# Kernel tuning notes

Hardware: AMD Instinct MI355X
Metric: run time of the kernel (lower is better)

Reference implementation:

```python
import jax, jax.numpy as jnp
import numpy as np

B, H, W = 16, 544, 960
DISP_MAX = 64.0


def setup_inputs() -> dict:
    key = jax.random.key(0)
    k1, k2, k3, k4 = jax.random.split(key, 4)
    dl = jax.random.uniform(k1, (B, 1, H, W), dtype=jnp.float32) * DISP_MAX
    seg_r = jax.random.normal(k2, (B, 1, H, W), dtype=jnp.float32)
    dlgt = jax.random.uniform(k3, (B, H, W), dtype=jnp.float32) * DISP_MAX
    lgt = jax.random.normal(k4, (B, 1, H, W), dtype=jnp.float32)
    return {"dl": dl, "seg_r": seg_r, "dlgt": dlgt, "lgt": lgt}


def _warp(x, disp):
    """Disparity warp: sample x at (h, w - disp) with horizontal bilinear
    interpolation and zeros padding (grid_sample equivalent; y is untouched
    so the vertical weights collapse to 1)."""
    Bc, C, Hc, Wc = x.shape
    cols = jnp.arange(Wc, dtype=x.dtype)  # [W]
    sx = cols[None, None, None, :] - disp  # [B,1,H,W] sampling x-coord
    x0 = jnp.floor(sx)
    wx = sx - x0  # fractional part, carries grad wrt disp
    x0i = x0.astype(jnp.int32)
    x1i = x0i + 1
    v0m = ((x0i >= 0) & (x0i < Wc)).astype(x.dtype)
    v1m = ((x1i >= 0) & (x1i < Wc)).astype(x.dtype)
    x0c = jnp.clip(x0i, 0, Wc - 1)
    x1c = jnp.clip(x1i, 0, Wc - 1)
    # gather along width; C == 1 broadcasts against disp's channel dim
    g0 = jnp.take_along_axis(x, jnp.broadcast_to(x0c, x.shape), axis=-1)
    g1 = jnp.take_along_axis(x, jnp.broadcast_to(x1c, x.shape), axis=-1)
    return (1.0 - wx) * g0 * v0m + wx * g1 * v1m


def _smooth_l1(d):
    ad = jnp.abs(d)
    return jnp.where(ad < 1.0, 0.5 * d * d, ad - 0.5)


def reference(dl, seg_r, dlgt, lgt):
    mask = lgt > 0  # [B,1,H,W] bool
    mf = mask.astype(dl.dtype)
    cnt = mf.sum()
    recon_l = jax.nn.sigmoid(_warp(seg_r, dl))
    # masked-mean smooth L1 == mean over boolean-selected elements
    loss_recon = (_smooth_l1(recon_l - lgt) * mf).sum() / cnt
    loss = (_smooth_l1(dl - dlgt[:, None, :, :]) * mf).sum() / cnt
    loss = jnp.where(jnp.isnan(loss), jnp.zeros_like(loss), loss)
    return loss + 0.5 * loss_recon
```

## Files before the change

kernel.cpp:

```cpp
#include <hip/hip_runtime.h>
#include <math.h>

#define W 960
#define NTOT (16 * 544 * 960)
#define N4 (NTOT / 4)
#define TPB 256
#define NBLOCKS 2048

typedef float vfloat4 __attribute__((ext_vector_type(4)));

__device__ __forceinline__ float smooth_l1f(float d) {
    float ad = fabsf(d);
    return ad < 1.0f ? 0.5f * d * d : ad - 0.5f;
}

__global__ __launch_bounds__(TPB) void loss_kernel(
    const float* __restrict__ dl,
    const float* __restrict__ seg_r,
    const float* __restrict__ dlgt,
    const float* __restrict__ lgt,
    double* __restrict__ ws)
{
    const int tid = threadIdx.x;
    float cnt = 0.f, s_loss = 0.f, s_recon = 0.f;

    for (int i4 = blockIdx.x * TPB + tid; i4 < N4; i4 += NBLOCKS * TPB) {
        int i  = i4 << 2;
        int w0 = i % W;
        const float* __restrict__ row = seg_r + (i - w0);

        vfloat4 d4 = __builtin_nontemporal_load((const vfloat4*)dl   + i4);
        vfloat4 l4 = __builtin_nontemporal_load((const vfloat4*)lgt  + i4);
        vfloat4 t4 = __builtin_nontemporal_load((const vfloat4*)dlgt + i4);

        #pragma unroll
        for (int k = 0; k < 4; ++k) {
            float lv = l4[k];
            float m = lv > 0.f ? 1.f : 0.f;
            cnt += m;
            float d = d4[k];
            s_loss += m * smooth_l1f(d - t4[k]);

            float sx  = (float)(w0 + k) - d;
            float x0f = floorf(sx);
            float wx  = sx - x0f;
            int x0 = (int)x0f;
            int x1 = x0 + 1;
            float m0 = (x0 >= 0 && x0 < W) ? 1.f : 0.f;
            float m1 = (x1 >= 0 && x1 < W) ? 1.f : 0.f;
            int x0c = min(max(x0, 0), W - 1);
            int x1c = min(max(x1, 0), W - 1);
            float g0 = row[x0c] * m0;
            float g1 = row[x1c] * m1;
            float wv = fmaf(wx, g1 - g0, g0);
            float recon = 1.f / (1.f + __expf(-wv));
            s_recon += m * smooth_l1f(recon - lv);
        }
    }

    double dc = (double)cnt, dlo = (double)s_loss, dre = (double)s_recon;
    for (int off = 32; off > 0; off >>= 1) {
        dc  += __shfl_down(dc,  off, 64);
        dlo += __shfl_down(dlo, off, 64);
        dre += __shfl_down(dre, off, 64);
    }
    __shared__ double sh[3][TPB / 64];
    int lane = tid & 63, wid = tid >> 6;
    if (lane == 0) { sh[0][wid] = dc; sh[1][wid] = dlo; sh[2][wid] = dre; }
    __syncthreads();

    if (tid == 0) {
        double c = 0, l = 0, r = 0;
        #pragma unroll
        for (int j = 0; j < TPB / 64; ++j) { c += sh[0][j]; l += sh[1][j]; r += sh[2][j]; }
        double* slot = ws + blockIdx.x * 4;
        slot[0] = c; slot[1] = l; slot[2] = r;
    }
}

__global__ __launch_bounds__(256) void finalize_kernel(
    const double* __restrict__ ws, float* __restrict__ out)
{
    double c = 0, l = 0, r = 0;
    for (int i = threadIdx.x; i < NBLOCKS; i += 256) {
        const double* slot = ws + i * 4;
        c += slot[0]; l += slot[1]; r += slot[2];
    }
    for (int off = 32; off > 0; off >>= 1) {
        c += __shfl_down(c, off, 64);
        l += __shfl_down(l, off, 64);
        r += __shfl_down(r, off, 64);
    }
    __shared__ double sh[3][4];
    int lane = threadIdx.x & 63, wid = threadIdx.x >> 6;
    if (lane == 0) { sh[0][wid] = c; sh[1][wid] = l; sh[2][wid] = r; }
    __syncthreads();
    if (threadIdx.x == 0) {
        double cc = 0, ll = 0, rr = 0;
        #pragma unroll
        for (int j = 0; j < 4; ++j) { cc += sh[0][j]; ll += sh[1][j]; rr += sh[2][j]; }
        double loss = ll / cc;
        if (isnan(loss)) loss = 0.0;
        out[0] = (float)(loss + 0.5 * (rr / cc));
    }
}

extern "C" void kernel_launch(void* const* d_in, const int* in_sizes, int n_in,
                              void* d_out, int out_size, void* d_ws, size_t ws_size,
                              hipStream_t stream) {
    const float* dl    = (const float*)d_in[0];
    const float* seg_r = (const float*)d_in[1];
    const float* dlgt  = (const float*)d_in[2];
    const float* lgt   = (const float*)d_in[3];
    double* ws = (double*)d_ws;

    loss_kernel<<<NBLOCKS, TPB, 0, stream>>>(dl, seg_r, dlgt, lgt, ws);
    finalize_kernel<<<1, 256, 0, stream>>>(ws, (float*)d_out);
}
```

Measured before the change: 149.1 us.

## Stage seg_r rows in LDS with one wave per row for warp gathers

Each wave now owns one image row and copies that seg_r row into shared memory, so the bilinear gathers read LDS instead of scattered global/cache loads. The grid-stride flat loop becomes a fixed per-row mapping with 2176 blocks, and the two gathers use one clamped adjacent pair with selects in place of two independent clamps. The main loads drop from float4 nontemporal to scalar coalesced loads, which may raise the instruction count, and the larger block count changes how the reduction is partitioned.

```diff
diff --git a/kernel.cpp b/kernel.cpp
--- a/kernel.cpp
+++ b/kernel.cpp
@@ -2,10 +2,9 @@
 #include <math.h>
 
 #define W 960
-#define NTOT (16 * 544 * 960)
-#define N4 (NTOT / 4)
+#define NROWS (16 * 544)
 #define TPB 256
-#define NBLOCKS 2048
+#define NBLOCKS (NROWS / 4)
 
 typedef float vfloat4 __attribute__((ext_vector_type(4)));
 
@@ -21,41 +20,49 @@
     const float* __restrict__ lgt,
     double* __restrict__ ws)
 {
-    const int tid = threadIdx.x;
+    __shared__ float srow[4][W];
+    __shared__ double sh[3][4];
+    const int tid  = threadIdx.x;
+    const int lane = tid & 63;
+    const int wave = tid >> 6;
+    const int rb   = (blockIdx.x * 4 + wave) * W;
+
+    #pragma unroll
+    for (int j = 0; j < 4; ++j) {
+        int idx4 = lane + 64 * j;
+        if (idx4 < 240)
+            *(vfloat4*)&srow[wave][idx4 << 2] = *(const vfloat4*)(seg_r + rb + (idx4 << 2));
+    }
+
+    const float* __restrict__ srw = srow[wave];
     float cnt = 0.f, s_loss = 0.f, s_recon = 0.f;
 
-    for (int i4 = blockIdx.x * TPB + tid; i4 < N4; i4 += NBLOCKS * TPB) {
-        int i  = i4 << 2;
-        int w0 = i % W;
-        const float* __restrict__ row = seg_r + (i - w0);
+    #pragma unroll
+    for (int j = 0; j < 15; ++j) {
+        int col = lane + 64 * j;
+        float d  = dl  [rb + col];
+        float lv = lgt [rb + col];
+        float tv = dlgt[rb + col];
 
-        vfloat4 d4 = __builtin_nontemporal_load((const vfloat4*)dl   + i4);
-        vfloat4 l4 = __builtin_nontemporal_load((const vfloat4*)lgt  + i4);
-        vfloat4 t4 = __builtin_nontemporal_load((const vfloat4*)dlgt + i4);
+        float m = lv > 0.f ? 1.f : 0.f;
+        cnt += m;
+        s_loss += m * smooth_l1f(d - tv);
 
-        #pragma unroll
-        for (int k = 0; k < 4; ++k) {
-            float lv = l4[k];
-            float m = lv > 0.f ? 1.f : 0.f;
-            cnt += m;
-            float d = d4[k];
-            s_loss += m * smooth_l1f(d - t4[k]);
-
-            float sx  = (float)(w0 + k) - d;
-            float x0f = floorf(sx);
-            float wx  = sx - x0f;
-            int x0 = (int)x0f;
-            int x1 = x0 + 1;
-            float m0 = (x0 >= 0 && x0 < W) ? 1.f : 0.f;
-            float m1 = (x1 >= 0 && x1 < W) ? 1.f : 0.f;
-            int x0c = min(max(x0, 0), W - 1);
-            int x1c = min(max(x1, 0), W - 1);
-            float g0 = row[x0c] * m0;
-            float g1 = row[x1c] * m1;
-            float wv = fmaf(wx, g1 - g0, g0);
-            float recon = 1.f / (1.f + __expf(-wv));
-            s_recon += m * smooth_l1f(recon - lv);
-        }
+        float sx  = (float)col - d;
+        float x0f = floorf(sx);
+        float wx  = sx - x0f;
+        int x0 = (int)x0f;
+        int xb = min(max(x0, 0), W - 2);
+        float p0 = srw[xb];
+        float p1 = srw[xb + 1];
+        bool  c  = (x0 == xb);
+        float m0 = (x0 >= 0) ? 1.f : 0.f;
+        float m1 = (x0 >= -1 && x0 <= W - 2) ? 1.f : 0.f;
+        float g0 = (c ? p0 : p1) * m0;
+        float g1 = (c ? p1 : p0) * m1;
+        float wv = fmaf(wx, g1 - g0, g0);
+        float recon = 1.f / (1.f + __expf(-wv));
+        s_recon += m * smooth_l1f(recon - lv);
     }
 
     double dc = (double)cnt, dlo = (double)s_loss, dre = (double)s_recon;
@@ -64,15 +71,13 @@
         dlo += __shfl_down(dlo, off, 64);
         dre += __shfl_down(dre, off, 64);
     }
-    __shared__ double sh[3][TPB / 64];
-    int lane = tid & 63, wid = tid >> 6;
-    if (lane == 0) { sh[0][wid] = dc; sh[1][wid] = dlo; sh[2][wid] = dre; }
+    if (lane == 0) { sh[0][wave] = dc; sh[1][wave] = dlo; sh[2][wave] = dre; }
     __syncthreads();
 
     if (tid == 0) {
         double c = 0, l = 0, r = 0;
         #pragma unroll
-        for (int j = 0; j < TPB / 64; ++j) { c += sh[0][j]; l += sh[1][j]; r += sh[2][j]; }
+        for (int j = 0; j < 4; ++j) { c += sh[0][j]; l += sh[1][j]; r += sh[2][j]; }
         double* slot = ws + blockIdx.x * 4;
         slot[0] = c; slot[1] = l; slot[2] = r;
     }
```

New measurement: 153.2 us. 1.03x slower.
